# Kernel tuning notes

Hardware: AMD Instinct MI355X
Metric: run time of the kernel (lower is better)

The kernel has to match this reference:

```python
import jax, jax.numpy as jnp
import numpy as np

N_NODES = 50000
N_EDGES = 800000
D = 128          # embed_dim
H = 8            # heads
C = D // H       # per-head channels
F = 512          # ff_hidden_dim
LN_EPS = 1e-5
NEG_SLOPE = 0.2  # PyG GATConv default negative_slope


def _layernorm(x, g, b):
    mu = jnp.mean(x, axis=-1, keepdims=True)
    var = jnp.mean(jnp.square(x - mu), axis=-1, keepdims=True)
    return (x - mu) * jax.lax.rsqrt(var + LN_EPS) * g + b


def _gat_conv(x, edge_index, W, att_src, att_dst, bias):
    # PyG GATConv (concat=True, add_self_loops=True, shared lin for src/dst)
    N = x.shape[0]
    xl = (x @ W.T).reshape(N, H, C)                 # [N,H,C]
    a_s = jnp.sum(xl * att_src, axis=-1)            # [N,H]
    a_d = jnp.sum(xl * att_dst, axis=-1)            # [N,H]
    loops = jnp.arange(N)
    src = jnp.concatenate([edge_index[0], loops])   # [E+N]
    dst = jnp.concatenate([edge_index[1], loops])
    e = jax.nn.leaky_relu(a_s[src] + a_d[dst], NEG_SLOPE)  # [E+N,H]
    # segment softmax over incoming edges per destination node
    m = jax.ops.segment_max(e, dst, num_segments=N)
    m = jnp.where(jnp.isfinite(m), m, jnp.zeros_like(m))
    ex = jnp.exp(e - m[dst])
    s = jax.ops.segment_sum(ex, dst, num_segments=N)
    alpha = ex / (s[dst] + 1e-16)                   # [E+N,H]
    msg = xl[src] * alpha[:, :, None]               # [E+N,H,C]
    out = jax.ops.segment_sum(msg, dst, num_segments=N)  # [N,H,C]
    return out.reshape(N, H * C) + bias


def setup_inputs() -> dict:
    key = jax.random.key(0)
    ks = jax.random.split(key, 12)
    sc_d = 1.0 / np.sqrt(D)
    sc_f = 1.0 / np.sqrt(F)
    return {
        "x": jax.random.normal(ks[0], (N_NODES, D), dtype=jnp.float32),
        "virtual_edge_index": jax.random.randint(ks[1], (2, N_EDGES), 0, N_NODES, dtype=jnp.int64),
        "W_gat": jax.random.normal(ks[2], (H * C, D), dtype=jnp.float32) * sc_d,
        "att_src": jax.random.normal(ks[3], (H, C), dtype=jnp.float32) * sc_d,
        "att_dst": jax.random.normal(ks[4], (H, C), dtype=jnp.float32) * sc_d,
        "bias_gat": jnp.zeros((H * C,), dtype=jnp.float32),
        "W1": jax.random.normal(ks[5], (F, D), dtype=jnp.float32) * sc_d,
        "b1": jnp.zeros((F,), dtype=jnp.float32),
        "W2": jax.random.normal(ks[6], (D, F), dtype=jnp.float32) * sc_f,
        "b2": jnp.zeros((D,), dtype=jnp.float32),
        "g1": jnp.ones((D,), dtype=jnp.float32),
        "beta1": jnp.zeros((D,), dtype=jnp.float32),
        "g2": jnp.ones((D,), dtype=jnp.float32),
        "beta2": jnp.zeros((D,), dtype=jnp.float32),
    }


def reference(x, virtual_edge_index, W_gat, att_src, att_dst, bias_gat,
              W1, b1, W2, b2, g1, beta1, g2, beta2):
    h_gat = _gat_conv(x, virtual_edge_index, W_gat, att_src, att_dst, bias_gat)
    h = _layernorm(x + h_gat, g1, beta1)
    h_ff = jax.nn.relu(h @ W1.T + b1) @ W2.T + b2
    return _layernorm(h + h_ff, g2, beta2)
```

## Files before the change

### kernel.cpp

```cpp
#include <hip/hip_runtime.h>
#include <hip/hip_bf16.h>

#define N_NODES 50000
#define N_EDGES 800000
#define N_TOT   850000
#define DIM 128
#define HEADS 8
#define CH 16
#define FF 512
#define LN_EPS 1e-5f
#define NEG_SLOPE 0.2f

typedef __bf16 bf16x8 __attribute__((ext_vector_type(8)));
typedef float f32x4 __attribute__((ext_vector_type(4)));

__device__ __forceinline__ float bfr2f(unsigned short u) {
  return __uint_as_float(((unsigned)u) << 16);
}
__device__ __forceinline__ unsigned short f2bfr(float f) {
  __hip_bfloat16 h = __float2bfloat16(f);
  return *(unsigned short*)&h;
}
__device__ __forceinline__ float bf2f(__hip_bfloat16 h) { return __bfloat162float(h); }
__device__ __forceinline__ __hip_bfloat16 f2bf(float f) { return __float2bfloat16(f); }

__device__ __forceinline__ bf16x8 ldcvt8(const float* __restrict__ p) {
  const float4 a = ((const float4*)p)[0];
  const float4 b = ((const float4*)p)[1];
  bf16x8 r;
  r[0] = (__bf16)a.x; r[1] = (__bf16)a.y; r[2] = (__bf16)a.z; r[3] = (__bf16)a.w;
  r[4] = (__bf16)b.x; r[5] = (__bf16)b.y; r[6] = (__bf16)b.z; r[7] = (__bf16)b.w;
  return r;
}
__device__ __forceinline__ void load8f(const float* __restrict__ p, float* v) {
  const float4 a = ((const float4*)p)[0];
  const float4 b = ((const float4*)p)[1];
  v[0]=a.x; v[1]=a.y; v[2]=a.z; v[3]=a.w; v[4]=b.x; v[5]=b.y; v[6]=b.z; v[7]=b.w;
}

__device__ __forceinline__ int ld_src(const int* ei, int mode, int e) {
  int v = mode ? ei[2 * e] : ei[e];
  return min(max(v, 0), N_NODES - 1);
}
__device__ __forceinline__ int ld_dst(const int* ei, int mode, int e) {
  int v = mode ? ei[2 * (N_EDGES + e)] : ei[N_EDGES + e];
  return min(max(v, 0), N_NODES - 1);
}

__global__ __launch_bounds__(256) void k_setup(const float* __restrict__ Wg,
                                               const float* __restrict__ W1,
                                               const float* __restrict__ W2,
                                               __hip_bfloat16* __restrict__ wb,
                                               const int* __restrict__ ei,
                                               int* __restrict__ flag,
                                               int* __restrict__ dz) {
  int i = blockIdx.x * 256 + threadIdx.x;
  if (i < 16384)       wb[i] = f2bf(Wg[i]);
  else if (i < 81920)  wb[i] = f2bf(W1[i - 16384]);
  else if (i < 147456) wb[i] = f2bf(W2[i - 81920]);
  if (i < 100096) dz[i] = 0;
  if (i == 0) {
    int any = 0;
    for (int k = 1; k < 64; k += 2) any |= ei[k];
    *flag = (any == 0) ? 1 : 0;
  }
}

__global__ __launch_bounds__(256) void k_xl(const float* __restrict__ x,
                                            const __hip_bfloat16* __restrict__ Wgb,
                                            __hip_bfloat16* __restrict__ xl) {
  int w = (blockIdx.x * blockDim.x + threadIdx.x) >> 6;
  if (w >= 3125 * 2) return;
  int l = threadIdx.x & 63, quad = l >> 4, r = l & 15;
  int strip = w >> 1, cc = w & 1;
  const __bf16* wb = (const __bf16*)Wgb;
  f32x4 acc[4];
#pragma unroll
  for (int t = 0; t < 4; ++t) acc[t] = (f32x4){0.f, 0.f, 0.f, 0.f};
  int arow = strip * 16 + r;
  bf16x8 af[4];
#pragma unroll
  for (int kk = 0; kk < 4; ++kk) af[kk] = ldcvt8(x + arow * DIM + kk * 32 + quad * 8);
#pragma unroll
  for (int kk = 0; kk < 4; ++kk) {
    bf16x8 bfr[4];
#pragma unroll
    for (int t = 0; t < 4; ++t)
      bfr[t] = *(const bf16x8*)(wb + (cc * 64 + t * 16 + r) * DIM + kk * 32 + quad * 8);
#pragma unroll
    for (int t = 0; t < 4; ++t)
      acc[t] = __builtin_amdgcn_mfma_f32_16x16x32_bf16(af[kk], bfr[t], acc[t], 0, 0, 0);
  }
#pragma unroll
  for (int t = 0; t < 4; ++t)
#pragma unroll
    for (int j = 0; j < 4; ++j) {
      int row = strip * 16 + quad * 4 + j;
      int col = cc * 64 + t * 16 + r;
      xl[row * DIM + col] = f2bf(acc[t][j]);
    }
}

__global__ __launch_bounds__(256) void k_score(const __hip_bfloat16* __restrict__ xl,
                                               const float* __restrict__ att_s,
                                               const float* __restrict__ att_d,
                                               float* __restrict__ a_s, float* __restrict__ a_d) {
  int t = blockIdx.x * 256 + threadIdx.x;
  if (t >= N_NODES * HEADS) return;
  int n = t >> 3, h = t & 7;
  const __hip_bfloat16* p = xl + n * DIM + h * CH;
  float s = 0.f, d = 0.f;
#pragma unroll
  for (int c = 0; c < CH; ++c) {
    float v = bf2f(p[c]);
    s += v * att_s[h * CH + c];
    d += v * att_d[h * CH + c];
  }
  a_s[t] = s; a_d[t] = d;
}

__global__ __launch_bounds__(256) void k_hist(const int* __restrict__ ei, const int* __restrict__ flag,
                                              int* __restrict__ deg) {
  int e = blockIdx.x * 256 + threadIdx.x;
  if (e < N_EDGES) atomicAdd(&deg[ld_dst(ei, *flag, e)], 1);
}

__global__ __launch_bounds__(1024) void k_scan(const int* __restrict__ deg, int* __restrict__ offs) {
  __shared__ int wtot[16];
  __shared__ int wbase[16];
  __shared__ int running_s;
  int tid = threadIdx.x, wv = tid >> 6, ln = tid & 63;
  if (tid == 0) running_s = 0;
  __syncthreads();
  for (int base = 0; base < N_NODES; base += 4096) {
    int i0 = base + tid * 4;
    int v0 = 0, v1 = 0, v2 = 0, v3 = 0;
    if (i0 + 3 < N_NODES) {
      int4 dv = *(const int4*)(deg + i0);
      v0 = dv.x + 1; v1 = dv.y + 1; v2 = dv.z + 1; v3 = dv.w + 1;
    } else {
      if (i0 + 0 < N_NODES) v0 = deg[i0 + 0] + 1;
      if (i0 + 1 < N_NODES) v1 = deg[i0 + 1] + 1;
      if (i0 + 2 < N_NODES) v2 = deg[i0 + 2] + 1;
      if (i0 + 3 < N_NODES) v3 = deg[i0 + 3] + 1;
    }
    int tt = v0 + v1 + v2 + v3;
    int xsc = tt;
#pragma unroll
    for (int off = 1; off < 64; off <<= 1) {
      int t = __shfl_up(xsc, off);
      if (ln >= off) xsc += t;
    }
    if (ln == 63) wtot[wv] = xsc;
    __syncthreads();
    if (wv == 0) {
      int t = (ln < 16) ? wtot[ln] : 0;
#pragma unroll
      for (int off = 1; off < 16; off <<= 1) {
        int u = __shfl_up(t, off);
        if (ln >= off) t += u;
      }
      if (ln < 16) wbase[ln] = t;
    }
    __syncthreads();
    int run0 = running_s;
    int excl = run0 + ((wv == 0) ? 0 : wbase[wv - 1]) + xsc - tt;
    if (i0 + 0 < N_NODES) offs[i0 + 0] = excl;
    excl += v0;
    if (i0 + 1 < N_NODES) offs[i0 + 1] = excl;
    excl += v1;
    if (i0 + 2 < N_NODES) offs[i0 + 2] = excl;
    excl += v2;
    if (i0 + 3 < N_NODES) offs[i0 + 3] = excl;
    __syncthreads();
    if (tid == 1023) running_s = run0 + wbase[15];
  }
  __syncthreads();
  if (tid == 0) offs[N_NODES] = running_s;
}

__global__ __launch_bounds__(256) void k_scatter(const int* __restrict__ ei, const int* __restrict__ flag,
                                                 const int* __restrict__ offs,
                                                 int* __restrict__ fill, int* __restrict__ eid,
                                                 int* __restrict__ did) {
  int e = blockIdx.x * 256 + threadIdx.x;
  if (e < N_NODES) { int p = offs[e]; eid[p] = e; did[p] = e; }
  if (e < N_EDGES) {
    int m = *flag;
    int d = ld_dst(ei, m, e);
    int p = offs[d] + 1 + atomicAdd(&fill[d], 1);
    eid[p] = ld_src(ei, m, e);
    did[p] = d;
  }
}

__global__ __launch_bounds__(256) void k_escore(const int* __restrict__ eid, const int* __restrict__ did,
                                                const float* __restrict__ a_s, const float* __restrict__ a_d,
                                                unsigned short* __restrict__ ex) {
  int p = blockIdx.x * 256 + threadIdx.x;
  if (p >= N_TOT) return;
  int s = eid[p], d = did[p];
  float as8[8], ad8[8];
  load8f(a_s + s * 8, as8);
  load8f(a_d + d * 8, ad8);
  unsigned int o[4];
#pragma unroll
  for (int k = 0; k < 4; ++k) {
    float v0 = as8[2 * k] + ad8[2 * k];
    v0 = v0 > 0.f ? v0 : NEG_SLOPE * v0;
    float v1 = as8[2 * k + 1] + ad8[2 * k + 1];
    v1 = v1 > 0.f ? v1 : NEG_SLOPE * v1;
    unsigned short e0 = f2bfr(__expf(v0));
    unsigned short e1 = f2bfr(__expf(v1));
    o[k] = (unsigned)e0 | ((unsigned)e1 << 16);
  }
  *(uint4*)(ex + p * 8) = make_uint4(o[0], o[1], o[2], o[3]);
}

__global__ __launch_bounds__(256) void k_attn(const int* __restrict__ eid, const int* __restrict__ offs,
                                              const unsigned short* __restrict__ ex,
                                              const __hip_bfloat16* __restrict__ xl,
                                              const float* __restrict__ x,
                                              const float* __restrict__ bias,
                                              const float* __restrict__ g1,
                                              const float* __restrict__ be1,
                                              __hip_bfloat16* __restrict__ h1out) {
  int wv = threadIdx.x >> 6, l = threadIdx.x & 63;
  int n = blockIdx.x * 4 + wv;
  int start = offs[n], end = offs[n + 1];

  float sme = 0.f;
  int flat1 = end * 8;
  for (int q = start * 8 + l; q < flat1; q += 64) sme += bfr2f(ex[q]);
  sme += __shfl_xor(sme, 8);
  sme += __shfl_xor(sme, 16);
  sme += __shfl_xor(sme, 32);
  float smh = __shfl(sme, l >> 3);
  float inv = 1.f / (smh + 1e-16f);

  int h = l >> 3;
  const unsigned short* xlu = (const unsigned short*)xl;
  float A0 = 0.f, A1 = 0.f, B0 = 0.f, B1 = 0.f, C0 = 0.f, C1 = 0.f, D0 = 0.f, D1 = 0.f;
  int p = start;
  for (; p + 4 <= end; p += 4) {
    int s0 = eid[p], s1 = eid[p + 1], s2 = eid[p + 2], s3 = eid[p + 3];
    float w0 = bfr2f(ex[(p)     * 8 + h]);
    float w1 = bfr2f(ex[(p + 1) * 8 + h]);
    float w2 = bfr2f(ex[(p + 2) * 8 + h]);
    float w3 = bfr2f(ex[(p + 3) * 8 + h]);
    ushort2 u0 = *(const ushort2*)(xlu + s0 * DIM + 2 * l);
    ushort2 u1 = *(const ushort2*)(xlu + s1 * DIM + 2 * l);
    ushort2 u2 = *(const ushort2*)(xlu + s2 * DIM + 2 * l);
    ushort2 u3 = *(const ushort2*)(xlu + s3 * DIM + 2 * l);
    A0 += w0 * bfr2f(u0.x); A1 += w0 * bfr2f(u0.y);
    B0 += w1 * bfr2f(u1.x); B1 += w1 * bfr2f(u1.y);
    C0 += w2 * bfr2f(u2.x); C1 += w2 * bfr2f(u2.y);
    D0 += w3 * bfr2f(u3.x); D1 += w3 * bfr2f(u3.y);
  }
  for (; p < end; ++p) {
    int s = eid[p];
    float wq = bfr2f(ex[p * 8 + h]);
    ushort2 u = *(const ushort2*)(xlu + s * DIM + 2 * l);
    A0 += wq * bfr2f(u.x); A1 += wq * bfr2f(u.y);
  }
  float acc0 = ((A0 + B0) + (C0 + D0)) * inv;
  float acc1 = ((A1 + B1) + (C1 + D1)) * inv;

  float2 xv = *(const float2*)(x + n * DIM + 2 * l);
  float2 bv = *(const float2*)(bias + 2 * l);
  float v0 = acc0 + bv.x + xv.x;
  float v1 = acc1 + bv.y + xv.y;
  float s2 = v0 + v1;
  for (int off = 32; off >= 1; off >>= 1) s2 += __shfl_xor(s2, off);
  float mu = s2 * (1.f / 128.f);
  float d0 = v0 - mu, d1 = v1 - mu;
  float q = d0 * d0 + d1 * d1;
  for (int off = 32; off >= 1; off >>= 1) q += __shfl_xor(q, off);
  float rs = rsqrtf(q * (1.f / 128.f) + LN_EPS);
  float2 gv = *(const float2*)(g1 + 2 * l);
  float2 bev = *(const float2*)(be1 + 2 * l);
  ushort2 o;
  o.x = f2bfr(d0 * rs * gv.x + bev.x);
  o.y = f2bfr(d1 * rs * gv.y + bev.y);
  *(ushort2*)((unsigned short*)h1out + n * DIM + 2 * l) = o;
}

#define LDSP 520
__global__ __launch_bounds__(256) void k_ffn(const __hip_bfloat16* __restrict__ h1,
                                             const __hip_bfloat16* __restrict__ W1b,
                                             const float* __restrict__ b1,
                                             const __hip_bfloat16* __restrict__ W2b,
                                             const float* __restrict__ b2,
                                             const float* __restrict__ g2,
                                             const float* __restrict__ be2,
                                             float* __restrict__ out) {
  __shared__ __bf16 hid[32 * LDSP];
  __shared__ float ps[4][2][16], pq[4][2][16];
  int wv = threadIdx.x >> 6, l = threadIdx.x & 63, quad = l >> 4, r = l & 15;
  int base = blockIdx.x * 32;
  const __bf16* h1b = (const __bf16*)h1;
  const __bf16* w1 = (const __bf16*)W1b;
  const __bf16* w2 = (const __bf16*)W2b;

  bf16x8 bn[2][4];
#pragma unroll
  for (int kk = 0; kk < 4; ++kk) {
    bn[0][kk] = *(const bf16x8*)(h1b + (base + r) * DIM + kk * 32 + quad * 8);
    bn[1][kk] = *(const bf16x8*)(h1b + (base + 16 + r) * DIM + kk * 32 + quad * 8);
  }
  f32x4 acc1[8][2];
#pragma unroll
  for (int tm = 0; tm < 8; ++tm)
#pragma unroll
    for (int tn = 0; tn < 2; ++tn) acc1[tm][tn] = (f32x4){0.f, 0.f, 0.f, 0.f};
#pragma unroll
  for (int kk = 0; kk < 4; ++kk) {
    bf16x8 wf[8];
#pragma unroll
    for (int tm = 0; tm < 8; ++tm)
      wf[tm] = *(const bf16x8*)(w1 + (wv * 128 + tm * 16 + r) * DIM + kk * 32 + quad * 8);
#pragma unroll
    for (int tm = 0; tm < 8; ++tm) {
      acc1[tm][0] = __builtin_amdgcn_mfma_f32_16x16x32_bf16(wf[tm], bn[0][kk], acc1[tm][0], 0, 0, 0);
      acc1[tm][1] = __builtin_amdgcn_mfma_f32_16x16x32_bf16(wf[tm], bn[1][kk], acc1[tm][1], 0, 0, 0);
    }
  }
#pragma unroll
  for (int tm = 0; tm < 8; ++tm) {
    int f0 = wv * 128 + tm * 16 + quad * 4;
    float4 bb = *(const float4*)(b1 + f0);
#pragma unroll
    for (int tn = 0; tn < 2; ++tn) {
      int node = tn * 16 + r;
      ushort4 o;
      o.x = f2bfr(fmaxf(acc1[tm][tn][0] + bb.x, 0.f));
      o.y = f2bfr(fmaxf(acc1[tm][tn][1] + bb.y, 0.f));
      o.z = f2bfr(fmaxf(acc1[tm][tn][2] + bb.z, 0.f));
      o.w = f2bfr(fmaxf(acc1[tm][tn][3] + bb.w, 0.f));
      *(ushort4*)&hid[node * LDSP + f0] = o;
    }
  }
  __syncthreads();

  f32x4 acc2[2][2];
#pragma unroll
  for (int s = 0; s < 2; ++s)
#pragma unroll
    for (int tn = 0; tn < 2; ++tn) acc2[s][tn] = (f32x4){0.f, 0.f, 0.f, 0.f};
#pragma unroll
  for (int k2 = 0; k2 < 8; ++k2) {
    int ka = 2 * k2, kb = 2 * k2 + 1;
    bf16x8 a0 = *(const bf16x8*)&hid[(r) * LDSP + ka * 32 + quad * 8];
    bf16x8 a1 = *(const bf16x8*)&hid[(16 + r) * LDSP + ka * 32 + quad * 8];
    bf16x8 a0b = *(const bf16x8*)&hid[(r) * LDSP + kb * 32 + quad * 8];
    bf16x8 a1b = *(const bf16x8*)&hid[(16 + r) * LDSP + kb * 32 + quad * 8];
    bf16x8 wa[2], wbq[2];
#pragma unroll
    for (int tn = 0; tn < 2; ++tn) {
      wa[tn]  = *(const bf16x8*)(w2 + (wv * 32 + tn * 16 + r) * FF + ka * 32 + quad * 8);
      wbq[tn] = *(const bf16x8*)(w2 + (wv * 32 + tn * 16 + r) * FF + kb * 32 + quad * 8);
    }
#pragma unroll
    for (int tn = 0; tn < 2; ++tn) {
      acc2[0][tn] = __builtin_amdgcn_mfma_f32_16x16x32_bf16(a0, wa[tn], acc2[0][tn], 0, 0, 0);
      acc2[1][tn] = __builtin_amdgcn_mfma_f32_16x16x32_bf16(a1, wa[tn], acc2[1][tn], 0, 0, 0);
    }
#pragma unroll
    for (int tn = 0; tn < 2; ++tn) {
      acc2[0][tn] = __builtin_amdgcn_mfma_f32_16x16x32_bf16(a0b, wbq[tn], acc2[0][tn], 0, 0, 0);
      acc2[1][tn] = __builtin_amdgcn_mfma_f32_16x16x32_bf16(a1b, wbq[tn], acc2[1][tn], 0, 0, 0);
    }
  }
#pragma unroll
  for (int s = 0; s < 2; ++s)
#pragma unroll
    for (int tn = 0; tn < 2; ++tn) {
      int col = wv * 32 + tn * 16 + r;
      float b2c = b2[col];
#pragma unroll
      for (int j = 0; j < 4; ++j)
        acc2[s][tn][j] += b2c + bf2f(h1[(base + s * 16 + quad * 4 + j) * DIM + col]);
    }
#pragma unroll
  for (int s = 0; s < 2; ++s)
#pragma unroll
    for (int j = 0; j < 4; ++j) {
      float sm = acc2[s][0][j] + acc2[s][1][j];
      float qm = acc2[s][0][j] * acc2[s][0][j] + acc2[s][1][j] * acc2[s][1][j];
      sm += __shfl_xor(sm, 1); sm += __shfl_xor(sm, 2); sm += __shfl_xor(sm, 4); sm += __shfl_xor(sm, 8);
      qm += __shfl_xor(qm, 1); qm += __shfl_xor(qm, 2); qm += __shfl_xor(qm, 4); qm += __shfl_xor(qm, 8);
      if (r == j) { ps[wv][s][quad * 4 + j] = sm; pq[wv][s][quad * 4 + j] = qm; }
    }
  __syncthreads();
#pragma unroll
  for (int s = 0; s < 2; ++s)
#pragma unroll
    for (int j = 0; j < 4; ++j) {
      int row16 = quad * 4 + j;
      float st = (ps[0][s][row16] + ps[1][s][row16]) + (ps[2][s][row16] + ps[3][s][row16]);
      float qt = (pq[0][s][row16] + pq[1][s][row16]) + (pq[2][s][row16] + pq[3][s][row16]);
      float mu = st * (1.f / 128.f);
      float var = qt * (1.f / 128.f) - mu * mu;
      float rs = rsqrtf(var + LN_EPS);
      int grow = base + s * 16 + row16;
      if (grow < N_NODES) {
#pragma unroll
        for (int tn = 0; tn < 2; ++tn) {
          int col = wv * 32 + tn * 16 + r;
          out[grow * DIM + col] = (acc2[s][tn][j] - mu) * rs * g2[col] + be2[col];
        }
      }
    }
}

#define OFF_XL     0u
#define SZ_XL      (N_NODES * DIM * 2u)
#define OFF_AS     (OFF_XL + SZ_XL)
#define SZ_AS      (N_NODES * HEADS * 4u)
#define OFF_AD     (OFF_AS + SZ_AS)
#define OFF_DEG    (OFF_AD + SZ_AS)
#define SZ_DEG     200192u
#define OFF_FILL   (OFF_DEG + SZ_DEG)
#define OFF_OFFS   (OFF_FILL + SZ_DEG)
#define SZ_OFFS    200448u
#define OFF_FLAG   (OFF_OFFS + SZ_OFFS)
#define OFF_EID    (OFF_FLAG + 256u)
#define SZ_EID     3400192u
#define OFF_DID    (OFF_EID + SZ_EID)
#define OFF_EX     (OFF_DID + SZ_EID)
#define SZ_EX      13600768u
#define OFF_H1     (OFF_EX + SZ_EX)
#define SZ_H1      (50016u * DIM * 2u)
#define OFF_WB     (OFF_H1 + SZ_H1)

extern "C" void kernel_launch(void* const* d_in, const int* in_sizes, int n_in,
                              void* d_out, int out_size, void* d_ws, size_t ws_size,
                              hipStream_t stream) {
  const float* x     = (const float*)d_in[0];
  const int*   ei    = (const int*)d_in[1];
  const float* Wg    = (const float*)d_in[2];
  const float* att_s = (const float*)d_in[3];
  const float* att_d = (const float*)d_in[4];
  const float* bias  = (const float*)d_in[5];
  const float* W1    = (const float*)d_in[6];
  const float* b1    = (const float*)d_in[7];
  const float* W2    = (const float*)d_in[8];
  const float* b2    = (const float*)d_in[9];
  const float* g1    = (const float*)d_in[10];
  const float* be1   = (const float*)d_in[11];
  const float* g2    = (const float*)d_in[12];
  const float* be2   = (const float*)d_in[13];

  char* ws = (char*)d_ws;
  __hip_bfloat16* xl     = (__hip_bfloat16*)(ws + OFF_XL);
  float*          a_s    = (float*)(ws + OFF_AS);
  float*          a_d    = (float*)(ws + OFF_AD);
  int*            deg    = (int*)(ws + OFF_DEG);
  int*            fill   = (int*)(ws + OFF_FILL);
  int*            offs   = (int*)(ws + OFF_OFFS);
  int*            flag   = (int*)(ws + OFF_FLAG);
  int*            eid    = (int*)(ws + OFF_EID);
  int*            did    = (int*)(ws + OFF_DID);
  unsigned short* ex     = (unsigned short*)(ws + OFF_EX);
  __hip_bfloat16* h1     = (__hip_bfloat16*)(ws + OFF_H1);
  __hip_bfloat16* wbuf   = (__hip_bfloat16*)(ws + OFF_WB);
  __hip_bfloat16* Wgb    = wbuf;
  __hip_bfloat16* W1b    = wbuf + 16384;
  __hip_bfloat16* W2b    = wbuf + 81920;
  float*          out    = (float*)d_out;

  k_setup  <<<576,   256, 0, stream>>>(Wg, W1, W2, wbuf, ei, flag, deg);
  k_xl     <<<1563,  256, 0, stream>>>(x, Wgb, xl);
  k_score  <<<1563,  256, 0, stream>>>(xl, att_s, att_d, a_s, a_d);
  k_hist   <<<3125,  256, 0, stream>>>(ei, flag, deg);
  k_scan   <<<1,    1024, 0, stream>>>(deg, offs);
  k_scatter<<<3125,  256, 0, stream>>>(ei, flag, offs, fill, eid, did);
  k_escore <<<3321,  256, 0, stream>>>(eid, did, a_s, a_d, ex);
  k_attn   <<<12500, 256, 0, stream>>>(eid, offs, ex, xl, x, bias, g1, be1, h1);
  k_ffn    <<<1563,  256, 0, stream>>>(h1, W1b, b1, W2b, b2, g2, be2, out);
}
```

Baseline: 356.8 us.

## Split FFN work across eight waves and stage residual rows in LDS

The FFN kernel now runs with 512 threads per block instead of 256. Each wave computes half as many hidden features in the first GEMM and one 16-column output slice in the second GEMM, which halves per-wave accumulator registers and gives each block more waves to hide latency. The h1 tile is also copied into shared memory so the residual add reads LDS instead of doing scattered global bf16 loads. The cost is more LDS per block and a wider LayerNorm partial-sum reduction across eight waves.

```diff
diff --git a/kernel.cpp b/kernel.cpp
--- a/kernel.cpp
+++ b/kernel.cpp
@@ -286,7 +286,8 @@
 }
 
 #define LDSP 520
-__global__ __launch_bounds__(256) void k_ffn(const __hip_bfloat16* __restrict__ h1,
+#define LDSR 136
+__global__ __launch_bounds__(512) void k_ffn(const __hip_bfloat16* __restrict__ h1,
                                              const __hip_bfloat16* __restrict__ W1b,
                                              const float* __restrict__ b1,
                                              const __hip_bfloat16* __restrict__ W2b,
@@ -295,7 +296,8 @@
                                              const float* __restrict__ be2,
                                              float* __restrict__ out) {
   __shared__ __bf16 hid[32 * LDSP];
-  __shared__ float ps[4][2][16], pq[4][2][16];
+  __shared__ __bf16 h1s[32 * LDSR];
+  __shared__ float ps[8][2][16], pq[8][2][16];
   int wv = threadIdx.x >> 6, l = threadIdx.x & 63, quad = l >> 4, r = l & 15;
   int base = blockIdx.x * 32;
   const __bf16* h1b = (const __bf16*)h1;
@@ -308,26 +310,31 @@
     bn[0][kk] = *(const bf16x8*)(h1b + (base + r) * DIM + kk * 32 + quad * 8);
     bn[1][kk] = *(const bf16x8*)(h1b + (base + 16 + r) * DIM + kk * 32 + quad * 8);
   }
-  f32x4 acc1[8][2];
-#pragma unroll
-  for (int tm = 0; tm < 8; ++tm)
+  if (wv < 2) {
+#pragma unroll
+    for (int kk = 0; kk < 4; ++kk)
+      *(bf16x8*)&h1s[(wv * 16 + r) * LDSR + kk * 32 + quad * 8] = bn[wv][kk];
+  }
+  f32x4 acc1[4][2];
+#pragma unroll
+  for (int tm = 0; tm < 4; ++tm)
 #pragma unroll
     for (int tn = 0; tn < 2; ++tn) acc1[tm][tn] = (f32x4){0.f, 0.f, 0.f, 0.f};
 #pragma unroll
   for (int kk = 0; kk < 4; ++kk) {
-    bf16x8 wf[8];
-#pragma unroll
-    for (int tm = 0; tm < 8; ++tm)
-      wf[tm] = *(const bf16x8*)(w1 + (wv * 128 + tm * 16 + r) * DIM + kk * 32 + quad * 8);
-#pragma unroll
-    for (int tm = 0; tm < 8; ++tm) {
+    bf16x8 wf[4];
+#pragma unroll
+    for (int tm = 0; tm < 4; ++tm)
+      wf[tm] = *(const bf16x8*)(w1 + (wv * 64 + tm * 16 + r) * DIM + kk * 32 + quad * 8);
+#pragma unroll
+    for (int tm = 0; tm < 4; ++tm) {
       acc1[tm][0] = __builtin_amdgcn_mfma_f32_16x16x32_bf16(wf[tm], bn[0][kk], acc1[tm][0], 0, 0, 0);
       acc1[tm][1] = __builtin_amdgcn_mfma_f32_16x16x32_bf16(wf[tm], bn[1][kk], acc1[tm][1], 0, 0, 0);
     }
   }
 #pragma unroll
-  for (int tm = 0; tm < 8; ++tm) {
-    int f0 = wv * 128 + tm * 16 + quad * 4;
+  for (int tm = 0; tm < 4; ++tm) {
+    int f0 = wv * 64 + tm * 16 + quad * 4;
     float4 bb = *(const float4*)(b1 + f0);
 #pragma unroll
     for (int tn = 0; tn < 2; ++tn) {
@@ -342,51 +349,30 @@
   }
   __syncthreads();
 
-  f32x4 acc2[2][2];
+  int col = wv * 16 + r;
+  f32x4 acc2[2];
+  acc2[0] = (f32x4){0.f, 0.f, 0.f, 0.f};
+  acc2[1] = (f32x4){0.f, 0.f, 0.f, 0.f};
+#pragma unroll
+  for (int kk = 0; kk < 16; ++kk) {
+    bf16x8 a0 = *(const bf16x8*)&hid[(r) * LDSP + kk * 32 + quad * 8];
+    bf16x8 a1 = *(const bf16x8*)&hid[(16 + r) * LDSP + kk * 32 + quad * 8];
+    bf16x8 wq = *(const bf16x8*)(w2 + col * FF + kk * 32 + quad * 8);
+    acc2[0] = __builtin_amdgcn_mfma_f32_16x16x32_bf16(a0, wq, acc2[0], 0, 0, 0);
+    acc2[1] = __builtin_amdgcn_mfma_f32_16x16x32_bf16(a1, wq, acc2[1], 0, 0, 0);
+  }
+  float b2c = b2[col], g2c = g2[col], be2c = be2[col];
 #pragma unroll
   for (int s = 0; s < 2; ++s)
 #pragma unroll
-    for (int tn = 0; tn < 2; ++tn) acc2[s][tn] = (f32x4){0.f, 0.f, 0.f, 0.f};
-#pragma unroll
-  for (int k2 = 0; k2 < 8; ++k2) {
-    int ka = 2 * k2, kb = 2 * k2 + 1;
-    bf16x8 a0 = *(const bf16x8*)&hid[(r) * LDSP + ka * 32 + quad * 8];
-    bf16x8 a1 = *(const bf16x8*)&hid[(16 + r) * LDSP + ka * 32 + quad * 8];
-    bf16x8 a0b = *(const bf16x8*)&hid[(r) * LDSP + kb * 32 + quad * 8];
-    bf16x8 a1b = *(const bf16x8*)&hid[(16 + r) * LDSP + kb * 32 + quad * 8];
-    bf16x8 wa[2], wbq[2];
-#pragma unroll
-    for (int tn = 0; tn < 2; ++tn) {
-      wa[tn]  = *(const bf16x8*)(w2 + (wv * 32 + tn * 16 + r) * FF + ka * 32 + quad * 8);
-      wbq[tn] = *(const bf16x8*)(w2 + (wv * 32 + tn * 16 + r) * FF + kb * 32 + quad * 8);
-    }
-#pragma unroll
-    for (int tn = 0; tn < 2; ++tn) {
-      acc2[0][tn] = __builtin_amdgcn_mfma_f32_16x16x32_bf16(a0, wa[tn], acc2[0][tn], 0, 0, 0);
-      acc2[1][tn] = __builtin_amdgcn_mfma_f32_16x16x32_bf16(a1, wa[tn], acc2[1][tn], 0, 0, 0);
-    }
-#pragma unroll
-    for (int tn = 0; tn < 2; ++tn) {
-      acc2[0][tn] = __builtin_amdgcn_mfma_f32_16x16x32_bf16(a0b, wbq[tn], acc2[0][tn], 0, 0, 0);
-      acc2[1][tn] = __builtin_amdgcn_mfma_f32_16x16x32_bf16(a1b, wbq[tn], acc2[1][tn], 0, 0, 0);
-    }
-  }
+    for (int j = 0; j < 4; ++j)
+      acc2[s][j] += b2c + bf2f(*(const __hip_bfloat16*)&h1s[(s * 16 + quad * 4 + j) * LDSR + col]);
 #pragma unroll
   for (int s = 0; s < 2; ++s)
 #pragma unroll
-    for (int tn = 0; tn < 2; ++tn) {
-      int col = wv * 32 + tn * 16 + r;
-      float b2c = b2[col];
-#pragma unroll
-      for (int j = 0; j < 4; ++j)
-        acc2[s][tn][j] += b2c + bf2f(h1[(base + s * 16 + quad * 4 + j) * DIM + col]);
-    }
-#pragma unroll
-  for (int s = 0; s < 2; ++s)
-#pragma unroll
     for (int j = 0; j < 4; ++j) {
-      float sm = acc2[s][0][j] + acc2[s][1][j];
-      float qm = acc2[s][0][j] * acc2[s][0][j] + acc2[s][1][j] * acc2[s][1][j];
+      float sm = acc2[s][j];
+      float qm = acc2[s][j] * acc2[s][j];
       sm += __shfl_xor(sm, 1); sm += __shfl_xor(sm, 2); sm += __shfl_xor(sm, 4); sm += __shfl_xor(sm, 8);
       qm += __shfl_xor(qm, 1); qm += __shfl_xor(qm, 2); qm += __shfl_xor(qm, 4); qm += __shfl_xor(qm, 8);
       if (r == j) { ps[wv][s][quad * 4 + j] = sm; pq[wv][s][quad * 4 + j] = qm; }
@@ -397,19 +383,16 @@
 #pragma unroll
     for (int j = 0; j < 4; ++j) {
       int row16 = quad * 4 + j;
-      float st = (ps[0][s][row16] + ps[1][s][row16]) + (ps[2][s][row16] + ps[3][s][row16]);
-      float qt = (pq[0][s][row16] + pq[1][s][row16]) + (pq[2][s][row16] + pq[3][s][row16]);
+      float st = ((ps[0][s][row16] + ps[1][s][row16]) + (ps[2][s][row16] + ps[3][s][row16]))
+               + ((ps[4][s][row16] + ps[5][s][row16]) + (ps[6][s][row16] + ps[7][s][row16]));
+      float qt = ((pq[0][s][row16] + pq[1][s][row16]) + (pq[2][s][row16] + pq[3][s][row16]))
+               + ((pq[4][s][row16] + pq[5][s][row16]) + (pq[6][s][row16] + pq[7][s][row16]));
       float mu = st * (1.f / 128.f);
       float var = qt * (1.f / 128.f) - mu * mu;
       float rs = rsqrtf(var + LN_EPS);
       int grow = base + s * 16 + row16;
-      if (grow < N_NODES) {
-#pragma unroll
-        for (int tn = 0; tn < 2; ++tn) {
-          int col = wv * 32 + tn * 16 + r;
-          out[grow * DIM + col] = (acc2[s][tn][j] - mu) * rs * g2[col] + be2[col];
-        }
-      }
+      if (grow < N_NODES)
+        out[grow * DIM + col] = (acc2[s][j] - mu) * rs * g2c + be2c;
     }
 }
 
@@ -477,5 +460,5 @@
   k_scatter<<<3125,  256, 0, stream>>>(ei, flag, offs, fill, eid, did);
   k_escore <<<3321,  256, 0, stream>>>(eid, did, a_s, a_d, ex);
   k_attn   <<<12500, 256, 0, stream>>>(eid, offs, ex, xl, x, bias, g1, be1, h1);
-  k_ffn    <<<1563,  256, 0, stream>>>(h1, W1b, b1, W2b, b2, g2, be2, out);
-}
+  k_ffn    <<<1563,  512, 0, stream>>>(h1, W1b, b1, W2b, b2, g2, be2, out);
+}
```

After: 393.0 us. 10.1% more time.
